# Kernel tuning notes

Hardware: AMD Instinct MI355X
Metric: run time of the kernel (lower is better)

## Reference

```python
import jax, jax.numpy as jnp
import numpy as np
import math

INPUT_SIZE = 512
HIDDEN_SIZE = 1024
BATCH = 64
SEQ = 512


def setup_inputs() -> dict:
    key = jax.random.key(0)
    ks = jax.random.split(key, 13)
    stdv = 1.0 / math.sqrt(HIDDEN_SIZE)
    def u(k, shape):
        return jax.random.uniform(k, shape, jnp.float32, -stdv, stdv)
    x = jax.random.normal(ks[0], (BATCH, SEQ, INPUT_SIZE), jnp.float32)
    return {
        "x": x,
        "U_i": u(ks[1], (INPUT_SIZE, HIDDEN_SIZE)), "V_i": u(ks[2], (HIDDEN_SIZE, HIDDEN_SIZE)), "b_i": u(ks[3], (HIDDEN_SIZE,)),
        "U_f": u(ks[4], (INPUT_SIZE, HIDDEN_SIZE)), "V_f": u(ks[5], (HIDDEN_SIZE, HIDDEN_SIZE)), "b_f": u(ks[6], (HIDDEN_SIZE,)),
        "U_c": u(ks[7], (INPUT_SIZE, HIDDEN_SIZE)), "V_c": u(ks[8], (HIDDEN_SIZE, HIDDEN_SIZE)), "b_c": u(ks[9], (HIDDEN_SIZE,)),
        "U_o": u(ks[10], (INPUT_SIZE, HIDDEN_SIZE)), "V_o": u(ks[11], (HIDDEN_SIZE, HIDDEN_SIZE)), "b_o": u(ks[12], (HIDDEN_SIZE,)),
    }


def reference(x, U_i, V_i, b_i, U_f, V_f, b_f, U_c, V_c, b_c, U_o, V_o, b_o):
    B, T, _ = x.shape
    H = V_i.shape[0]
    # Fuse the four input->gate matmuls into one wide GEMM over all timesteps.
    U = jnp.concatenate([U_i, U_f, U_c, U_o], axis=1)  # [I, 4H]
    V = jnp.concatenate([V_i, V_f, V_c, V_o], axis=1)  # [H, 4H]
    b = jnp.concatenate([b_i, b_f, b_c, b_o], axis=0)  # [4H]
    xU = jnp.einsum('bti,ig->tbg', x, U) + b           # [T, B, 4H]

    def step(carry, xu_t):
        h, c = carry
        gates = xu_t + h @ V                           # [B, 4H]
        i_t = jax.nn.sigmoid(gates[:, 0*H:1*H])
        f_t = jax.nn.sigmoid(gates[:, 1*H:2*H])
        g_t = jax.nn.sigmoid(gates[:, 2*H:3*H])  # NOTE: source uses sigmoid, not tanh
        o_t = jax.nn.sigmoid(gates[:, 3*H:4*H])
        c = f_t * c + i_t * g_t
        h = o_t * jnp.tanh(c)
        return (h, c), h

    h0 = jnp.zeros((B, H), x.dtype)
    c0 = jnp.zeros((B, H), x.dtype)
    (h_T, c_T), hs = jax.lax.scan(step, (h0, c0), xU)
    hidden_seq = jnp.transpose(hs, (1, 0, 2))          # [B, T, H]
    return hidden_seq, (h_T, c_T)
```

## Files before the change

### kernel.cpp

```cpp
#include <hip/hip_runtime.h>
#include <stdint.h>

#define B_  64
#define T_  512
#define I_  512
#define H_  1024
#define G4  4096
#define KW  1536

#define GROUPS 4
#define GBLK   64
#define MBR    16

#define LDS_BYTES 66048

typedef __attribute__((ext_vector_type(8))) short bf16x8;
typedef __attribute__((ext_vector_type(4))) float f32x4;

#define OFF_WT   ((size_t)0)
#define OFF_XB   ((size_t)(16u << 20))
#define OFF_HB   (OFF_XB + (size_t)33554432)
#define WS_NEED  (OFF_HB + (size_t)262144)

__device__ __forceinline__ unsigned short f2bf(float x) {
  unsigned u = __float_as_uint(x);
  u += 0x7FFFu + ((u >> 16) & 1u);
  return (unsigned short)(u >> 16);
}
__device__ __forceinline__ float sigm(float x) {
  return 1.0f / (1.0f + __expf(-x));
}

__global__ __launch_bounds__(256) void pack_w_kernel(
    const float* __restrict__ U0, const float* __restrict__ U1,
    const float* __restrict__ U2, const float* __restrict__ U3,
    const float* __restrict__ V0, const float* __restrict__ V1,
    const float* __restrict__ V2, const float* __restrict__ V3,
    short* __restrict__ Wt)
{
  __shared__ short sl[64][65];
  const int c0 = blockIdx.x * 64;
  const int k0 = blockIdx.y * 64;
  const int g  = c0 >> 10;
  const int h0 = c0 & 1023;
  const float* srcU = (g == 0 ? U0 : g == 1 ? U1 : g == 2 ? U2 : U3);
  const float* srcV = (g == 0 ? V0 : g == 1 ? V1 : g == 2 ? V2 : V3);
  const float* src  = (k0 < 512) ? (srcU + (size_t)k0 * H_)
                                 : (srcV + (size_t)(k0 - 512) * H_);
  const int tid = threadIdx.x;
  const int cl = tid & 63;
  const int r4 = tid >> 6;
  #pragma unroll
  for (int r = 0; r < 16; ++r) {
    const int kl = r * 4 + r4;
    sl[kl][cl] = (short)f2bf(src[(size_t)kl * H_ + h0 + cl]);
  }
  __syncthreads();
  #pragma unroll
  for (int r = 0; r < 16; ++r) {
    const int cl2 = r * 4 + r4;
    Wt[(size_t)(c0 + cl2) * KW + k0 + cl] = sl[cl][cl2];
  }
}

__global__ __launch_bounds__(256) void xcvt(
    const float* __restrict__ x, short* __restrict__ xb)
{
  const int nt = 524288;
  const int idx = blockIdx.x * 256 + threadIdx.x;
  #pragma unroll
  for (int i = 0; i < 8; ++i) {
    const int j = idx + i * nt;
    const float4 v = ((const float4*)x)[j];
    uint2 pk;
    pk.x = (unsigned)f2bf(v.x) | ((unsigned)f2bf(v.y) << 16);
    pk.y = (unsigned)f2bf(v.z) | ((unsigned)f2bf(v.w) << 16);
    ((uint2*)xb)[j] = pk;
  }
}

#define FR_ADDR(unit, slot) ((((unit) * 64) + ((slot) ^ ((unit) & 7))) * 8)

__global__ __launch_bounds__(512, 2) void lstm_rec(
    const short* __restrict__ Wt, const short* __restrict__ xb,
    const float* __restrict__ b0g, const float* __restrict__ b1g,
    const float* __restrict__ b2g, const float* __restrict__ b3g,
    short* __restrict__ hb, float* __restrict__ out)
{
  extern __shared__ char smem[];
  short* sh = (short*)smem;
  short* sx = (short*)(smem + 32768);
  float* gl = (float*)(smem + 49152);

  const int tid = threadIdx.x;
  const int blk = blockIdx.x;
  const int g   = blk >> 6;
  const int bi  = blk & 63;
  const int base = bi * 16;
  const int b0  = g * MBR;

  const int w = tid >> 6, l = tid & 63;
  const int kq = w & 3;
  const int np = w >> 2;
  const int cit = l & 15;
  const int l16 = l >> 4;
  const int slot_r = (cit << 2) | l16;

  bf16x8 vfr[2][8];
  bf16x8 ufr[2][4];
  #pragma unroll
  for (int n = 0; n < 2; ++n) {
    const int col = (np * 2 + n) * 1024 + base + cit;
    const short* wp = Wt + (size_t)col * KW;
    #pragma unroll
    for (int j = 0; j < 8; ++j)
      vfr[n][j] = *(const bf16x8*)(wp + 512 + kq * 256 + j * 32 + l16 * 8);
    #pragma unroll
    for (int j = 0; j < 4; ++j)
      ufr[n][j] = *(const bf16x8*)(wp + kq * 128 + j * 32 + l16 * 8);
  }

  const float* bias0 = (np == 0) ? b0g : b2g;
  const float* bias1 = (np == 0) ? b1g : b3g;
  const float bv0 = (kq == 0) ? bias0[base + cit] : 0.0f;
  const float bv1 = (kq == 0) ? bias1[base + cit] : 0.0f;

  const int crow = tid >> 4;
  const int ccj  = tid & 15;

  const int xr0_row = tid >> 6;
  const int xr1_row = 8 + (tid >> 6);
  const int x_k0 = (tid & 63) * 8;
  const int x_unit = x_k0 >> 5;
  const int xr0_addr = FR_ADDR(x_unit, (xr0_row << 2) | (tid & 3));
  const int xr1_addr = FR_ADDR(x_unit, (xr1_row << 2) | (tid & 3));
  const short* xsrc0 = xb + (size_t)(b0 + xr0_row) * T_ * I_ + x_k0;
  const short* xsrc1 = xb + (size_t)(b0 + xr1_row) * T_ * I_ + x_k0;

  float c_state = 0.0f;

  *(int4*)(sx + xr0_addr) = *(const int4*)(xsrc0);
  *(int4*)(sx + xr1_addr) = *(const int4*)(xsrc1);
  __syncthreads();
  f32x4 xacc0 = (f32x4){bv0, bv0, bv0, bv0};
  f32x4 xacc1 = (f32x4){bv1, bv1, bv1, bv1};
  #pragma unroll
  for (int j = 0; j < 4; ++j) {
    const bf16x8 xf = *(const bf16x8*)(sx + FR_ADDR(kq * 4 + j, slot_r));
    xacc0 = __builtin_amdgcn_mfma_f32_16x16x32_bf16(xf, ufr[0][j], xacc0, 0, 0, 0);
    xacc1 = __builtin_amdgcn_mfma_f32_16x16x32_bf16(xf, ufr[1][j], xacc1, 0, 0, 0);
  }
  int4 xr0 = *(const int4*)(xsrc0 + (size_t)1 * I_);
  int4 xr1 = *(const int4*)(xsrc1 + (size_t)1 * I_);

  for (int t = 0; t < T_; ++t) {
    {
      const unsigned expw = ((t >> 1) & 1) ? 0x00010001u : 0u;
      const short* hsrc = hb + ((size_t)(t & 1) * GROUPS + g) * (MBR * H_);
      int4 v0, v1, v2, v3;
      for (;;) {
        #define LDC(ii, vv) { \
          const short* p = hsrc + (size_t)((((ii) * 512 + tid) >> 7)) * H_ \
                           + ((((ii) * 512 + tid) & 127) * 8); \
          asm volatile("global_load_dwordx4 %0, %1, off sc0 sc1" : "=&v"(vv) : "v"(p)); }
        LDC(0, v0) LDC(1, v1) LDC(2, v2) LDC(3, v3)
        #undef LDC
        asm volatile("s_waitcnt vmcnt(0)" ::: "memory");
        __builtin_amdgcn_sched_barrier(0);
        #define XR(vv) (((unsigned)(vv).x ^ expw) | ((unsigned)(vv).y ^ expw) | \
                        ((unsigned)(vv).z ^ expw) | ((unsigned)(vv).w ^ expw))
        const unsigned diff = (XR(v0) | XR(v1) | XR(v2) | XR(v3)) & 0x00010001u;
        #undef XR
        if (__all(diff == 0u)) break;
        asm volatile("s_sleep 1" ::: "memory");
      }
      #define STC(ii, vv) { const int f = (ii) * 512 + tid; const int row = f >> 7; \
        const int k0s = (f & 127) * 8; \
        *(int4*)(sh + FR_ADDR(k0s >> 5, (row << 2) | ((k0s >> 3) & 3))) = vv; }
      STC(0, v0) STC(1, v1) STC(2, v2) STC(3, v3)
      #undef STC
    }
    __syncthreads();

    f32x4 acc0 = xacc0, acc1 = xacc1;
    #pragma unroll
    for (int j = 0; j < 8; ++j) {
      const bf16x8 af = *(const bf16x8*)(sh + FR_ADDR(kq * 8 + j, slot_r));
      acc0 = __builtin_amdgcn_mfma_f32_16x16x32_bf16(af, vfr[0][j], acc0, 0, 0, 0);
      acc1 = __builtin_amdgcn_mfma_f32_16x16x32_bf16(af, vfr[1][j], acc1, 0, 0, 0);
    }

    #pragma unroll
    for (int i = 0; i < 4; ++i) {
      gl[(l16 * 4 + i) * 260 + kq * 64 + (np * 2 + 0) * 16 + cit] = acc0[i];
      gl[(l16 * 4 + i) * 260 + kq * 64 + (np * 2 + 1) * 16 + cit] = acc1[i];
    }
    __syncthreads();

    if (tid < 256) {
      const float* gr = gl + crow * 260;
      float s[4];
      #pragma unroll
      for (int gate = 0; gate < 4; ++gate)
        s[gate] = gr[0 * 64 + gate * 16 + ccj] + gr[1 * 64 + gate * 16 + ccj]
                + gr[2 * 64 + gate * 16 + ccj] + gr[3 * 64 + gate * 16 + ccj];
      const float i_ = sigm(s[0]), f_ = sigm(s[1]), g_ = sigm(s[2]), o_ = sigm(s[3]);
      c_state = f_ * c_state + i_ * g_;
      const float hval = o_ * tanhf(c_state);
      if (t + 1 < T_) {
        unsigned hv = (unsigned)f2bf(hval);
        hv = (hv & ~1u) | (unsigned)(((t + 1) >> 1) & 1);
        short* hdst = hb + ((size_t)((t + 1) & 1) * GROUPS + g) * (MBR * H_)
                      + (size_t)crow * H_ + base + ccj;
        asm volatile("global_store_short %0, %1, off sc0 sc1" :: "v"(hdst), "v"(hv) : "memory");
      }
      out[((size_t)(b0 + crow) << 19) + (size_t)t * H_ + base + ccj] = hval;
      if (t == T_ - 1) {
        out[(size_t)B_ * T_ * H_ + (size_t)(b0 + crow) * H_ + base + ccj] = hval;
        out[(size_t)B_ * T_ * H_ + (size_t)B_ * H_ + (size_t)(b0 + crow) * H_ + base + ccj] = c_state;
      }
    }

    if (t + 1 < T_) {
      *(int4*)(sx + xr0_addr) = xr0;
      *(int4*)(sx + xr1_addr) = xr1;
      {
        const size_t tn = (size_t)((t + 2 < T_) ? t + 2 : T_ - 1);
        xr0 = *(const int4*)(xsrc0 + tn * I_);
        xr1 = *(const int4*)(xsrc1 + tn * I_);
      }
      __syncthreads();

      xacc0 = (f32x4){bv0, bv0, bv0, bv0};
      xacc1 = (f32x4){bv1, bv1, bv1, bv1};
      #pragma unroll
      for (int j = 0; j < 4; ++j) {
        const bf16x8 xf = *(const bf16x8*)(sx + FR_ADDR(kq * 4 + j, slot_r));
        xacc0 = __builtin_amdgcn_mfma_f32_16x16x32_bf16(xf, ufr[0][j], xacc0, 0, 0, 0);
        xacc1 = __builtin_amdgcn_mfma_f32_16x16x32_bf16(xf, ufr[1][j], xacc1, 0, 0, 0);
      }
    }
  }
}

extern "C" void kernel_launch(void* const* d_in, const int* in_sizes, int n_in,
                              void* d_out, int out_size, void* d_ws, size_t ws_size,
                              hipStream_t stream)
{
  const float* x  = (const float*)d_in[0];
  const float* U0 = (const float*)d_in[1];
  const float* Vg0 = (const float*)d_in[2];
  const float* bg0 = (const float*)d_in[3];
  const float* U1 = (const float*)d_in[4];
  const float* Vg1 = (const float*)d_in[5];
  const float* bg1 = (const float*)d_in[6];
  const float* U2 = (const float*)d_in[7];
  const float* Vg2 = (const float*)d_in[8];
  const float* bg2 = (const float*)d_in[9];
  const float* U3 = (const float*)d_in[10];
  const float* Vg3 = (const float*)d_in[11];
  const float* bg3 = (const float*)d_in[12];

  if (ws_size < WS_NEED) return;

  char* ws = (char*)d_ws;
  short* Wt = (short*)(ws + OFF_WT);
  short* xb = (short*)(ws + OFF_XB);
  short* hb = (short*)(ws + OFF_HB);

  (void)hipFuncSetAttribute((const void*)lstm_rec,
                      hipFuncAttributeMaxDynamicSharedMemorySize, LDS_BYTES);

  (void)hipMemsetAsync(ws + OFF_HB, 0x00, 131072, stream);
  (void)hipMemsetAsync(ws + OFF_HB + 131072, 0x01, 131072, stream);
  pack_w_kernel<<<dim3(64, 24), 256, 0, stream>>>(U0, U1, U2, U3, Vg0, Vg1, Vg2, Vg3, Wt);
  xcvt<<<dim3(2048), 256, 0, stream>>>(x, xb);
  lstm_rec<<<dim3(GROUPS * GBLK), 512, LDS_BYTES, stream>>>(
      Wt, xb, bg0, bg1, bg2, bg3, hb, (float*)d_out);
}
```

Measured before the change: 1.143 ms.

## Give each wave a private h tile to drop the block barrier before MFMA

Each wave now polls and loads only the part of the hidden state its own K-quarter needs, and writes it into a private LDS region. This removes the __syncthreads between the h load and the recurrent MFMA. A single-vector probe spin runs before the bulk eight-load read, and the sleep in the bulk retry grows. tanhf is replaced with an exp-based fast tanh. LDS use grows and the launch bound drops to one block per CU; each wave now loads its share redundantly (2x total h traffic), and fast_tanh may overflow to inf for large inputs.

Result: slower. 1.461 ms (+27.8%).

```diff
diff --git a/kernel.cpp b/kernel.cpp
--- a/kernel.cpp
+++ b/kernel.cpp
@@ -12,7 +12,7 @@
 #define GBLK   64
 #define MBR    16
 
-#define LDS_BYTES 66048
+#define LDS_BYTES 98560
 
 typedef __attribute__((ext_vector_type(8))) short bf16x8;
 typedef __attribute__((ext_vector_type(4))) float f32x4;
@@ -29,6 +29,10 @@
 }
 __device__ __forceinline__ float sigm(float x) {
   return 1.0f / (1.0f + __expf(-x));
+}
+__device__ __forceinline__ float fast_tanh(float x) {
+  const float e2 = __expf(2.0f * x);
+  return 1.0f - 2.0f / (e2 + 1.0f);
 }
 
 __global__ __launch_bounds__(256) void pack_w_kernel(
@@ -81,7 +85,7 @@
 
 #define FR_ADDR(unit, slot) ((((unit) * 64) + ((slot) ^ ((unit) & 7))) * 8)
 
-__global__ __launch_bounds__(512, 2) void lstm_rec(
+__global__ __launch_bounds__(512, 1) void lstm_rec(
     const short* __restrict__ Wt, const short* __restrict__ xb,
     const float* __restrict__ b0g, const float* __restrict__ b1g,
     const float* __restrict__ b2g, const float* __restrict__ b3g,
@@ -89,8 +93,8 @@
 {
   extern __shared__ char smem[];
   short* sh = (short*)smem;
-  short* sx = (short*)(smem + 32768);
-  float* gl = (float*)(smem + 49152);
+  short* sx = (short*)(smem + 65536);
+  float* gl = (float*)(smem + 81920);
 
   const int tid = threadIdx.x;
   const int blk = blockIdx.x;
@@ -105,6 +109,7 @@
   const int cit = l & 15;
   const int l16 = l >> 4;
   const int slot_r = (cit << 2) | l16;
+  short* shw = sh + w * 4096;
 
   bf16x8 vfr[2][8];
   bf16x8 ufr[2][4];
@@ -128,6 +133,11 @@
   const int crow = tid >> 4;
   const int ccj  = tid & 15;
 
+  const int prow = l >> 5;
+  const int pcolo = kq * 256 + (l & 31) * 8;
+  const int s_unit = (l >> 2) & 7;
+  const int s_ks = l & 3;
+
   const int xr0_row = tid >> 6;
   const int xr1_row = 8 + (tid >> 6);
   const int x_k0 = (tid & 63) * 8;
@@ -152,40 +162,51 @@
   }
   int4 xr0 = *(const int4*)(xsrc0 + (size_t)1 * I_);
   int4 xr1 = *(const int4*)(xsrc1 + (size_t)1 * I_);
+  __syncthreads();
 
   for (int t = 0; t < T_; ++t) {
     {
       const unsigned expw = ((t >> 1) & 1) ? 0x00010001u : 0u;
       const short* hsrc = hb + ((size_t)(t & 1) * GROUPS + g) * (MBR * H_);
-      int4 v0, v1, v2, v3;
+      const short* pb = hsrc + (size_t)prow * H_ + pcolo;
+      #define XR(vv) ((((unsigned)(vv).x ^ expw) | ((unsigned)(vv).y ^ expw) | \
+                       ((unsigned)(vv).z ^ expw) | ((unsigned)(vv).w ^ expw)) & 0x00010001u)
+      {
+        int4 pv;
+        for (;;) {
+          asm volatile("global_load_dwordx4 %0, %1, off sc0 sc1" : "=&v"(pv) : "v"(pb));
+          asm volatile("s_waitcnt vmcnt(0)" ::: "memory");
+          if (__all(XR(pv) == 0u)) break;
+          asm volatile("s_sleep 1" ::: "memory");
+        }
+      }
+      int4 v0, v1, v2, v3, v4, v5, v6, v7;
       for (;;) {
         #define LDC(ii, vv) { \
-          const short* p = hsrc + (size_t)((((ii) * 512 + tid) >> 7)) * H_ \
-                           + ((((ii) * 512 + tid) & 127) * 8); \
+          const short* p = hsrc + (size_t)(2 * (ii) + prow) * H_ + pcolo; \
           asm volatile("global_load_dwordx4 %0, %1, off sc0 sc1" : "=&v"(vv) : "v"(p)); }
         LDC(0, v0) LDC(1, v1) LDC(2, v2) LDC(3, v3)
+        LDC(4, v4) LDC(5, v5) LDC(6, v6) LDC(7, v7)
         #undef LDC
         asm volatile("s_waitcnt vmcnt(0)" ::: "memory");
         __builtin_amdgcn_sched_barrier(0);
-        #define XR(vv) (((unsigned)(vv).x ^ expw) | ((unsigned)(vv).y ^ expw) | \
-                        ((unsigned)(vv).z ^ expw) | ((unsigned)(vv).w ^ expw))
-        const unsigned diff = (XR(v0) | XR(v1) | XR(v2) | XR(v3)) & 0x00010001u;
-        #undef XR
+        const unsigned diff = XR(v0) | XR(v1) | XR(v2) | XR(v3)
+                            | XR(v4) | XR(v5) | XR(v6) | XR(v7);
         if (__all(diff == 0u)) break;
-        asm volatile("s_sleep 1" ::: "memory");
-      }
-      #define STC(ii, vv) { const int f = (ii) * 512 + tid; const int row = f >> 7; \
-        const int k0s = (f & 127) * 8; \
-        *(int4*)(sh + FR_ADDR(k0s >> 5, (row << 2) | ((k0s >> 3) & 3))) = vv; }
+        asm volatile("s_sleep 2" ::: "memory");
+      }
+      #undef XR
+      #define STC(ii, vv) { const int row = 2 * (ii) + prow; \
+        *(int4*)(shw + FR_ADDR(s_unit, (row << 2) | s_ks)) = vv; }
       STC(0, v0) STC(1, v1) STC(2, v2) STC(3, v3)
+      STC(4, v4) STC(5, v5) STC(6, v6) STC(7, v7)
       #undef STC
     }
-    __syncthreads();
 
     f32x4 acc0 = xacc0, acc1 = xacc1;
     #pragma unroll
     for (int j = 0; j < 8; ++j) {
-      const bf16x8 af = *(const bf16x8*)(sh + FR_ADDR(kq * 8 + j, slot_r));
+      const bf16x8 af = *(const bf16x8*)(shw + FR_ADDR(j, slot_r));
       acc0 = __builtin_amdgcn_mfma_f32_16x16x32_bf16(af, vfr[0][j], acc0, 0, 0, 0);
       acc1 = __builtin_amdgcn_mfma_f32_16x16x32_bf16(af, vfr[1][j], acc1, 0, 0, 0);
     }
@@ -206,7 +227,7 @@
                 + gr[2 * 64 + gate * 16 + ccj] + gr[3 * 64 + gate * 16 + ccj];
       const float i_ = sigm(s[0]), f_ = sigm(s[1]), g_ = sigm(s[2]), o_ = sigm(s[3]);
       c_state = f_ * c_state + i_ * g_;
-      const float hval = o_ * tanhf(c_state);
+      const float hval = o_ * fast_tanh(c_state);
       if (t + 1 < T_) {
         unsigned hv = (unsigned)f2bf(hval);
         hv = (hv & ~1u) | (unsigned)(((t + 1) >> 1) & 1);
```

## Interleave two batch groups per block with speculative h prefetch and narrower column slices

Applied to the files above, without the earlier changes.

Each block now owns 8 hidden columns for two 16-row batch groups and alternates between them, so the wait on one group's h exchange overlaps with computing the other. The h loads for the next half-step are issued speculatively before the barrier and checked afterwards, with a retry loop if the parity flags do not match. x is loaded straight into registers as MFMA fragments instead of going through LDS, tanh is replaced with an exp-based form, and the K dimension is split across all 8 waves. The kernel now runs at one block per CU with more LDS, and reloading h on a failed speculation costs extra memory traffic.

Result: slower. 3.029 ms (+165.0%).

```diff
diff --git a/kernel.cpp b/kernel.cpp
--- a/kernel.cpp
+++ b/kernel.cpp
@@ -5,14 +5,9 @@
 #define T_  512
 #define I_  512
 #define H_  1024
-#define G4  4096
 #define KW  1536
 
-#define GROUPS 4
-#define GBLK   64
-#define MBR    16
-
-#define LDS_BYTES 66048
+#define LDS_BYTES 98816
 
 typedef __attribute__((ext_vector_type(8))) short bf16x8;
 typedef __attribute__((ext_vector_type(4))) float f32x4;
@@ -29,6 +24,13 @@
 }
 __device__ __forceinline__ float sigm(float x) {
   return 1.0f / (1.0f + __expf(-x));
+}
+__device__ __forceinline__ float fast_tanh(float x) {
+  const float e2 = __expf(2.0f * x);
+  return 1.0f - 2.0f / (e2 + 1.0f);
+}
+__device__ __forceinline__ bf16x8 bc8(int4 v) {
+  union { int4 i; bf16x8 b; } u; u.i = v; return u.b;
 }
 
 __global__ __launch_bounds__(256) void pack_w_kernel(
@@ -80,166 +82,209 @@
 }
 
 #define FR_ADDR(unit, slot) ((((unit) * 64) + ((slot) ^ ((unit) & 7))) * 8)
-
-__global__ __launch_bounds__(512, 2) void lstm_rec(
+#define FOFF(f) ((((f) >> 7) * 1024) + (((f) & 127) * 8))
+#define SADR(f) FR_ADDR((((f) & 127) >> 2), ((((f) >> 7) << 2) | ((f) & 3)))
+
+#define XRD_(vv, ew) ((((unsigned)(vv).x ^ (ew)) | ((unsigned)(vv).y ^ (ew)) | \
+                       ((unsigned)(vv).z ^ (ew)) | ((unsigned)(vv).w ^ (ew))) & 0x00010001u)
+#define LDH(vv, p) asm volatile("global_load_dwordx4 %0, %1, off sc0 sc1" : "=&v"(vv) : "v"(p));
+#define LDX(vv, p) asm volatile("global_load_dwordx4 %0, %1, off" : "=&v"(vv) : "v"(p));
+
+#define RETRY_(hsrc, ew) \
+  for (;;) { \
+    LDH(sp0, (hsrc) + foff0) LDH(sp1, (hsrc) + foff1) \
+    LDH(sp2, (hsrc) + foff2) LDH(sp3, (hsrc) + foff3) \
+    asm volatile("s_waitcnt vmcnt(0)" ::: "memory"); \
+    __builtin_amdgcn_sched_barrier(0); \
+    if (__all((XRD_(sp0, ew) | XRD_(sp1, ew) | XRD_(sp2, ew) | XRD_(sp3, ew)) == 0u)) break; \
+    asm volatile("s_sleep 1" ::: "memory"); \
+  }
+
+#define HALF(SH, GL, HBG, XROW, B0, XACCA, XACCB, CST, HLAST, XVA, XVB, SPECHBG, SPECT, TCUR, DOCHK) \
+{ \
+  const unsigned ew = (((TCUR) >> 1) & 1) ? 0x00010001u : 0u; \
+  const short* hsrc = (HBG) + (((TCUR) & 1) ? 65536 : 0); \
+  bool ok = (DOCHK); \
+  if (ok) { \
+    asm volatile("s_waitcnt vmcnt(2)" ::: "memory"); \
+    __builtin_amdgcn_sched_barrier(0); \
+    ok = __all((XRD_(sp0, ew) | XRD_(sp1, ew) | XRD_(sp2, ew) | XRD_(sp3, ew)) == 0u); \
+  } \
+  if (!ok) { RETRY_(hsrc, ew) } \
+  *(int4*)((SH) + saddr0) = sp0; \
+  *(int4*)((SH) + saddr1) = sp1; \
+  *(int4*)((SH) + saddr2) = sp2; \
+  *(int4*)((SH) + saddr3) = sp3; \
+  { const int tn = ((TCUR) + 1 < T_) ? (TCUR) + 1 : T_ - 1; \
+    const short* xp = (XROW) + (size_t)tn * I_; \
+    LDX(XVA, xp) LDX(XVB, xp + 32) } \
+  { const short* ss = (SPECHBG) + (((SPECT) & 1) ? 65536 : 0); \
+    LDH(sp0, ss + foff0) LDH(sp1, ss + foff1) LDH(sp2, ss + foff2) LDH(sp3, ss + foff3) } \
+  __syncthreads(); \
+  f32x4 accA = XACCA, accB = XACCB; \
+  { \
+    bf16x8 af; \
+    af = *(const bf16x8*)((SH) + FR_ADDR(kqe * 4 + 0, slot_r)); \
+    accA = __builtin_amdgcn_mfma_f32_16x16x32_bf16(af, vfr0[0], accA, 0, 0, 0); \
+    accB = __builtin_amdgcn_mfma_f32_16x16x32_bf16(af, vfr1[0], accB, 0, 0, 0); \
+    af = *(const bf16x8*)((SH) + FR_ADDR(kqe * 4 + 1, slot_r)); \
+    accA = __builtin_amdgcn_mfma_f32_16x16x32_bf16(af, vfr0[1], accA, 0, 0, 0); \
+    accB = __builtin_amdgcn_mfma_f32_16x16x32_bf16(af, vfr1[1], accB, 0, 0, 0); \
+    af = *(const bf16x8*)((SH) + FR_ADDR(kqe * 4 + 2, slot_r)); \
+    accA = __builtin_amdgcn_mfma_f32_16x16x32_bf16(af, vfr0[2], accA, 0, 0, 0); \
+    accB = __builtin_amdgcn_mfma_f32_16x16x32_bf16(af, vfr1[2], accB, 0, 0, 0); \
+    af = *(const bf16x8*)((SH) + FR_ADDR(kqe * 4 + 3, slot_r)); \
+    accA = __builtin_amdgcn_mfma_f32_16x16x32_bf16(af, vfr0[3], accA, 0, 0, 0); \
+    accB = __builtin_amdgcn_mfma_f32_16x16x32_bf16(af, vfr1[3], accB, 0, 0, 0); \
+  } \
+  { \
+    (GL)[(l16 * 4 + 0) * 260 + cit * 8 + kqe] = accA[0]; \
+    (GL)[(l16 * 4 + 1) * 260 + cit * 8 + kqe] = accA[1]; \
+    (GL)[(l16 * 4 + 2) * 260 + cit * 8 + kqe] = accA[2]; \
+    (GL)[(l16 * 4 + 3) * 260 + cit * 8 + kqe] = accA[3]; \
+    (GL)[(l16 * 4 + 0) * 260 + (16 + cit) * 8 + kqe] = accB[0]; \
+    (GL)[(l16 * 4 + 1) * 260 + (16 + cit) * 8 + kqe] = accB[1]; \
+    (GL)[(l16 * 4 + 2) * 260 + (16 + cit) * 8 + kqe] = accB[2]; \
+    (GL)[(l16 * 4 + 3) * 260 + (16 + cit) * 8 + kqe] = accB[3]; \
+  } \
+  __syncthreads(); \
+  asm volatile("s_waitcnt vmcnt(4)" ::: "memory"); \
+  __builtin_amdgcn_sched_barrier(0); \
+  { \
+    const bf16x8 xf0 = bc8(XVA), xf1 = bc8(XVB); \
+    XACCA = (f32x4){bv0, bv0, bv0, bv0}; \
+    XACCB = (f32x4){bv1, bv1, bv1, bv1}; \
+    XACCA = __builtin_amdgcn_mfma_f32_16x16x32_bf16(xf0, ufr0[0], XACCA, 0, 0, 0); \
+    XACCA = __builtin_amdgcn_mfma_f32_16x16x32_bf16(xf1, ufr0[1], XACCA, 0, 0, 0); \
+    XACCB = __builtin_amdgcn_mfma_f32_16x16x32_bf16(xf0, ufr1[0], XACCB, 0, 0, 0); \
+    XACCB = __builtin_amdgcn_mfma_f32_16x16x32_bf16(xf1, ufr1[1], XACCB, 0, 0, 0); \
+  } \
+  if (l < 16) { \
+    const float* gr = (GL) + crow * 260; \
+    const f32x4 a0 = *(const f32x4*)(gr + ccol * 8); \
+    const f32x4 b0a = *(const f32x4*)(gr + ccol * 8 + 4); \
+    const f32x4 a1 = *(const f32x4*)(gr + 64 + ccol * 8); \
+    const f32x4 b1a = *(const f32x4*)(gr + 64 + ccol * 8 + 4); \
+    const f32x4 a2 = *(const f32x4*)(gr + 128 + ccol * 8); \
+    const f32x4 b2a = *(const f32x4*)(gr + 128 + ccol * 8 + 4); \
+    const f32x4 a3 = *(const f32x4*)(gr + 192 + ccol * 8); \
+    const f32x4 b3a = *(const f32x4*)(gr + 192 + ccol * 8 + 4); \
+    const float s0 = a0[0]+a0[1]+a0[2]+a0[3]+b0a[0]+b0a[1]+b0a[2]+b0a[3]; \
+    const float s1 = a1[0]+a1[1]+a1[2]+a1[3]+b1a[0]+b1a[1]+b1a[2]+b1a[3]; \
+    const float s2 = a2[0]+a2[1]+a2[2]+a2[3]+b2a[0]+b2a[1]+b2a[2]+b2a[3]; \
+    const float s3 = a3[0]+a3[1]+a3[2]+a3[3]+b3a[0]+b3a[1]+b3a[2]+b3a[3]; \
+    const float i_ = sigm(s0), f_ = sigm(s1), g_ = sigm(s2), o_ = sigm(s3); \
+    CST = f_ * CST + i_ * g_; \
+    const float hv = o_ * fast_tanh(CST); \
+    HLAST = hv; \
+    unsigned hu = (unsigned)f2bf(hv); \
+    hu = (hu & ~1u) | (unsigned)((((TCUR) + 1) >> 1) & 1); \
+    short* hd = (HBG) + ((((TCUR) + 1) & 1) ? 65536 : 0) + crow * 1024 + base8 + ccol; \
+    asm volatile("global_store_short %0, %1, off sc0 sc1" :: "v"(hd), "v"(hu) : "memory"); \
+    float* op = out + (((size_t)((B0) + crow)) << 19) + (size_t)(TCUR) * H_ + base8 + ccol; \
+    asm volatile("global_store_dword %0, %1, off" :: "v"(op), "v"(hv) : "memory"); \
+  } \
+}
+
+__global__ __launch_bounds__(512, 1) void lstm_rec(
     const short* __restrict__ Wt, const short* __restrict__ xb,
     const float* __restrict__ b0g, const float* __restrict__ b1g,
     const float* __restrict__ b2g, const float* __restrict__ b3g,
     short* __restrict__ hb, float* __restrict__ out)
 {
   extern __shared__ char smem[];
-  short* sh = (short*)smem;
-  short* sx = (short*)(smem + 32768);
-  float* gl = (float*)(smem + 49152);
+  short* shP = (short*)smem;
+  short* shQ = (short*)(smem + 32768);
+  float* glP = (float*)(smem + 65536);
+  float* glQ = (float*)(smem + 82176);
 
   const int tid = threadIdx.x;
   const int blk = blockIdx.x;
-  const int g   = blk >> 6;
-  const int bi  = blk & 63;
-  const int base = bi * 16;
-  const int b0  = g * MBR;
-
+  const int pair = blk >> 7;
+  const int bi = blk & 127;
+  const int base8 = bi * 8;
   const int w = tid >> 6, l = tid & 63;
-  const int kq = w & 3;
-  const int np = w >> 2;
-  const int cit = l & 15;
-  const int l16 = l >> 4;
+  const int kqe = w;
+  const int cit = l & 15, l16 = l >> 4;
   const int slot_r = (cit << 2) | l16;
-
-  bf16x8 vfr[2][8];
-  bf16x8 ufr[2][4];
-  #pragma unroll
-  for (int n = 0; n < 2; ++n) {
-    const int col = (np * 2 + n) * 1024 + base + cit;
-    const short* wp = Wt + (size_t)col * KW;
+  const int Pg = pair * 2, Qg = pair * 2 + 1;
+  const int b0P = Pg * 16, b0Q = Qg * 16;
+
+  short* hbP = hb + Pg * 16384;
+  short* hbQ = hb + Qg * 16384;
+
+  bf16x8 vfr0[4], vfr1[4], ufr0[2], ufr1[2];
+  float bv0, bv1;
+  {
+    const int g0 = cit >> 3, c8 = cit & 7;
+    const short* wpa = Wt + (size_t)(g0 * 1024 + base8 + c8) * KW;
+    const short* wpb = Wt + (size_t)((2 + g0) * 1024 + base8 + c8) * KW;
     #pragma unroll
-    for (int j = 0; j < 8; ++j)
-      vfr[n][j] = *(const bf16x8*)(wp + 512 + kq * 256 + j * 32 + l16 * 8);
+    for (int j = 0; j < 4; ++j) {
+      vfr0[j] = *(const bf16x8*)(wpa + 512 + kqe * 128 + j * 32 + l16 * 8);
+      vfr1[j] = *(const bf16x8*)(wpb + 512 + kqe * 128 + j * 32 + l16 * 8);
+    }
     #pragma unroll
-    for (int j = 0; j < 4; ++j)
-      ufr[n][j] = *(const bf16x8*)(wp + kq * 128 + j * 32 + l16 * 8);
-  }
-
-  const float* bias0 = (np == 0) ? b0g : b2g;
-  const float* bias1 = (np == 0) ? b1g : b3g;
-  const float bv0 = (kq == 0) ? bias0[base + cit] : 0.0f;
-  const float bv1 = (kq == 0) ? bias1[base + cit] : 0.0f;
-
-  const int crow = tid >> 4;
-  const int ccj  = tid & 15;
-
-  const int xr0_row = tid >> 6;
-  const int xr1_row = 8 + (tid >> 6);
-  const int x_k0 = (tid & 63) * 8;
-  const int x_unit = x_k0 >> 5;
-  const int xr0_addr = FR_ADDR(x_unit, (xr0_row << 2) | (tid & 3));
-  const int xr1_addr = FR_ADDR(x_unit, (xr1_row << 2) | (tid & 3));
-  const short* xsrc0 = xb + (size_t)(b0 + xr0_row) * T_ * I_ + x_k0;
-  const short* xsrc1 = xb + (size_t)(b0 + xr1_row) * T_ * I_ + x_k0;
-
-  float c_state = 0.0f;
-
-  *(int4*)(sx + xr0_addr) = *(const int4*)(xsrc0);
-  *(int4*)(sx + xr1_addr) = *(const int4*)(xsrc1);
-  __syncthreads();
-  f32x4 xacc0 = (f32x4){bv0, bv0, bv0, bv0};
-  f32x4 xacc1 = (f32x4){bv1, bv1, bv1, bv1};
-  #pragma unroll
-  for (int j = 0; j < 4; ++j) {
-    const bf16x8 xf = *(const bf16x8*)(sx + FR_ADDR(kq * 4 + j, slot_r));
-    xacc0 = __builtin_amdgcn_mfma_f32_16x16x32_bf16(xf, ufr[0][j], xacc0, 0, 0, 0);
-    xacc1 = __builtin_amdgcn_mfma_f32_16x16x32_bf16(xf, ufr[1][j], xacc1, 0, 0, 0);
-  }
-  int4 xr0 = *(const int4*)(xsrc0 + (size_t)1 * I_);
-  int4 xr1 = *(const int4*)(xsrc1 + (size_t)1 * I_);
+    for (int j = 0; j < 2; ++j) {
+      ufr0[j] = *(const bf16x8*)(wpa + kqe * 64 + j * 32 + l16 * 8);
+      ufr1[j] = *(const bf16x8*)(wpb + kqe * 64 + j * 32 + l16 * 8);
+    }
+    const float* bpa = g0 ? b1g : b0g;
+    const float* bpb = g0 ? b3g : b2g;
+    bv0 = (kqe == 0) ? bpa[base8 + c8] : 0.0f;
+    bv1 = (kqe == 0) ? bpb[base8 + c8] : 0.0f;
+  }
+
+  const int f0_ = tid, f1_ = 512 + tid, f2_ = 1024 + tid, f3_ = 1536 + tid;
+  const int foff0 = FOFF(f0_), foff1 = FOFF(f1_), foff2 = FOFF(f2_), foff3 = FOFF(f3_);
+  const int saddr0 = SADR(f0_), saddr1 = SADR(f1_), saddr2 = SADR(f2_), saddr3 = SADR(f3_);
+
+  const short* xrowP = xb + (size_t)(b0P + cit) * T_ * I_ + kqe * 64 + l16 * 8;
+  const short* xrowQ = xb + (size_t)(b0Q + cit) * T_ * I_ + kqe * 64 + l16 * 8;
+
+  const int crow = 2 * w + (l >> 3);
+  const int ccol = l & 7;
+
+  float cP = 0.0f, cQ = 0.0f, hlP = 0.0f, hlQ = 0.0f;
+  int4 sp0, sp1, sp2, sp3;
+  int4 xvP0, xvP1, xvQ0, xvQ1;
+  f32x4 xaccP0, xaccP1, xaccQ0, xaccQ1;
+
+  LDX(xvP0, xrowP) LDX(xvP1, xrowP + 32)
+  LDX(xvQ0, xrowQ) LDX(xvQ1, xrowQ + 32)
+  asm volatile("s_waitcnt vmcnt(0)" ::: "memory");
+  __builtin_amdgcn_sched_barrier(0);
+  {
+    const bf16x8 p0 = bc8(xvP0), p1 = bc8(xvP1), q0 = bc8(xvQ0), q1 = bc8(xvQ1);
+    xaccP0 = (f32x4){bv0, bv0, bv0, bv0};
+    xaccP1 = (f32x4){bv1, bv1, bv1, bv1};
+    xaccQ0 = (f32x4){bv0, bv0, bv0, bv0};
+    xaccQ1 = (f32x4){bv1, bv1, bv1, bv1};
+    xaccP0 = __builtin_amdgcn_mfma_f32_16x16x32_bf16(p0, ufr0[0], xaccP0, 0, 0, 0);
+    xaccP0 = __builtin_amdgcn_mfma_f32_16x16x32_bf16(p1, ufr0[1], xaccP0, 0, 0, 0);
+    xaccP1 = __builtin_amdgcn_mfma_f32_16x16x32_bf16(p0, ufr1[0], xaccP1, 0, 0, 0);
+    xaccP1 = __builtin_amdgcn_mfma_f32_16x16x32_bf16(p1, ufr1[1], xaccP1, 0, 0, 0);
+    xaccQ0 = __builtin_amdgcn_mfma_f32_16x16x32_bf16(q0, ufr0[0], xaccQ0, 0, 0, 0);
+    xaccQ0 = __builtin_amdgcn_mfma_f32_16x16x32_bf16(q1, ufr0[1], xaccQ0, 0, 0, 0);
+    xaccQ1 = __builtin_amdgcn_mfma_f32_16x16x32_bf16(q0, ufr1[0], xaccQ1, 0, 0, 0);
+    xaccQ1 = __builtin_amdgcn_mfma_f32_16x16x32_bf16(q1, ufr1[1], xaccQ1, 0, 0, 0);
+  }
 
   for (int t = 0; t < T_; ++t) {
-    {
-      const unsigned expw = ((t >> 1) & 1) ? 0x00010001u : 0u;
-      const short* hsrc = hb + ((size_t)(t & 1) * GROUPS + g) * (MBR * H_);
-      int4 v0, v1, v2, v3;
-      for (;;) {
-        #define LDC(ii, vv) { \
-          const short* p = hsrc + (size_t)((((ii) * 512 + tid) >> 7)) * H_ \
-                           + ((((ii) * 512 + tid) & 127) * 8); \
-          asm volatile("global_load_dwordx4 %0, %1, off sc0 sc1" : "=&v"(vv) : "v"(p)); }
-        LDC(0, v0) LDC(1, v1) LDC(2, v2) LDC(3, v3)
-        #undef LDC
-        asm volatile("s_waitcnt vmcnt(0)" ::: "memory");
-        __builtin_amdgcn_sched_barrier(0);
-        #define XR(vv) (((unsigned)(vv).x ^ expw) | ((unsigned)(vv).y ^ expw) | \
-                        ((unsigned)(vv).z ^ expw) | ((unsigned)(vv).w ^ expw))
-        const unsigned diff = (XR(v0) | XR(v1) | XR(v2) | XR(v3)) & 0x00010001u;
-        #undef XR
-        if (__all(diff == 0u)) break;
-        asm volatile("s_sleep 1" ::: "memory");
-      }
-      #define STC(ii, vv) { const int f = (ii) * 512 + tid; const int row = f >> 7; \
-        const int k0s = (f & 127) * 8; \
-        *(int4*)(sh + FR_ADDR(k0s >> 5, (row << 2) | ((k0s >> 3) & 3))) = vv; }
-      STC(0, v0) STC(1, v1) STC(2, v2) STC(3, v3)
-      #undef STC
-    }
-    __syncthreads();
-
-    f32x4 acc0 = xacc0, acc1 = xacc1;
-    #pragma unroll
-    for (int j = 0; j < 8; ++j) {
-      const bf16x8 af = *(const bf16x8*)(sh + FR_ADDR(kq * 8 + j, slot_r));
-      acc0 = __builtin_amdgcn_mfma_f32_16x16x32_bf16(af, vfr[0][j], acc0, 0, 0, 0);
-      acc1 = __builtin_amdgcn_mfma_f32_16x16x32_bf16(af, vfr[1][j], acc1, 0, 0, 0);
-    }
-
-    #pragma unroll
-    for (int i = 0; i < 4; ++i) {
-      gl[(l16 * 4 + i) * 260 + kq * 64 + (np * 2 + 0) * 16 + cit] = acc0[i];
-      gl[(l16 * 4 + i) * 260 + kq * 64 + (np * 2 + 1) * 16 + cit] = acc1[i];
-    }
-    __syncthreads();
-
-    if (tid < 256) {
-      const float* gr = gl + crow * 260;
-      float s[4];
-      #pragma unroll
-      for (int gate = 0; gate < 4; ++gate)
-        s[gate] = gr[0 * 64 + gate * 16 + ccj] + gr[1 * 64 + gate * 16 + ccj]
-                + gr[2 * 64 + gate * 16 + ccj] + gr[3 * 64 + gate * 16 + ccj];
-      const float i_ = sigm(s[0]), f_ = sigm(s[1]), g_ = sigm(s[2]), o_ = sigm(s[3]);
-      c_state = f_ * c_state + i_ * g_;
-      const float hval = o_ * tanhf(c_state);
-      if (t + 1 < T_) {
-        unsigned hv = (unsigned)f2bf(hval);
-        hv = (hv & ~1u) | (unsigned)(((t + 1) >> 1) & 1);
-        short* hdst = hb + ((size_t)((t + 1) & 1) * GROUPS + g) * (MBR * H_)
-                      + (size_t)crow * H_ + base + ccj;
-        asm volatile("global_store_short %0, %1, off sc0 sc1" :: "v"(hdst), "v"(hv) : "memory");
-      }
-      out[((size_t)(b0 + crow) << 19) + (size_t)t * H_ + base + ccj] = hval;
-      if (t == T_ - 1) {
-        out[(size_t)B_ * T_ * H_ + (size_t)(b0 + crow) * H_ + base + ccj] = hval;
-        out[(size_t)B_ * T_ * H_ + (size_t)B_ * H_ + (size_t)(b0 + crow) * H_ + base + ccj] = c_state;
-      }
-    }
-
-    if (t + 1 < T_) {
-      *(int4*)(sx + xr0_addr) = xr0;
-      *(int4*)(sx + xr1_addr) = xr1;
-      {
-        const size_t tn = (size_t)((t + 2 < T_) ? t + 2 : T_ - 1);
-        xr0 = *(const int4*)(xsrc0 + tn * I_);
-        xr1 = *(const int4*)(xsrc1 + tn * I_);
-      }
-      __syncthreads();
-
-      xacc0 = (f32x4){bv0, bv0, bv0, bv0};
-      xacc1 = (f32x4){bv1, bv1, bv1, bv1};
-      #pragma unroll
-      for (int j = 0; j < 4; ++j) {
-        const bf16x8 xf = *(const bf16x8*)(sx + FR_ADDR(kq * 4 + j, slot_r));
-        xacc0 = __builtin_amdgcn_mfma_f32_16x16x32_bf16(xf, ufr[0][j], xacc0, 0, 0, 0);
-        xacc1 = __builtin_amdgcn_mfma_f32_16x16x32_bf16(xf, ufr[1][j], xacc1, 0, 0, 0);
-      }
-    }
+    HALF(shP, glP, hbP, xrowP, b0P, xaccP0, xaccP1, cP, hlP, xvP0, xvP1, hbQ, t,     t, (t > 0))
+    HALF(shQ, glQ, hbQ, xrowQ, b0Q, xaccQ0, xaccQ1, cQ, hlQ, xvQ0, xvQ1, hbP, t + 1, t, true)
+  }
+
+  if (l < 16) {
+    const size_t fb = (size_t)B_ * T_ * H_;
+    float* p1 = out + fb + (size_t)(b0P + crow) * H_ + base8 + ccol;
+    float* p2 = out + fb + (size_t)B_ * H_ + (size_t)(b0P + crow) * H_ + base8 + ccol;
+    float* q1 = out + fb + (size_t)(b0Q + crow) * H_ + base8 + ccol;
+    float* q2 = out + fb + (size_t)B_ * H_ + (size_t)(b0Q + crow) * H_ + base8 + ccol;
+    asm volatile("global_store_dword %0, %1, off" :: "v"(p1), "v"(hlP) : "memory");
+    asm volatile("global_store_dword %0, %1, off" :: "v"(p2), "v"(cP) : "memory");
+    asm volatile("global_store_dword %0, %1, off" :: "v"(q1), "v"(hlQ) : "memory");
+    asm volatile("global_store_dword %0, %1, off" :: "v"(q2), "v"(cQ) : "memory");
   }
 }
 
@@ -275,6 +320,6 @@
   (void)hipMemsetAsync(ws + OFF_HB + 131072, 0x01, 131072, stream);
   pack_w_kernel<<<dim3(64, 24), 256, 0, stream>>>(U0, U1, U2, U3, Vg0, Vg1, Vg2, Vg3, Wt);
   xcvt<<<dim3(2048), 256, 0, stream>>>(x, xb);
-  lstm_rec<<<dim3(GROUPS * GBLK), 512, LDS_BYTES, stream>>>(
+  lstm_rec<<<dim3(256), 512, LDS_BYTES, stream>>>(
       Wt, xb, bg0, bg1, bg2, bg3, hb, (float*)d_out);
 }
```

## Halve recurrent block count with 32 hidden columns per block and faster gate reduction

Applied to the files above, without the earlier changes.

Each block now owns 32 hidden columns instead of 16, so the grid shrinks from 256 to 128 persistent blocks and each wave holds four weight-fragment sets in registers and issues four MFMA chains per step. The gate scratch layout is transposed so that all 512 threads do the cell update, each reading its four partial sums with one vector load. tanh is replaced by an exp-based approximation. The intent is to cut the number of blocks polling the global h buffer and spread per-step elementwise work over more threads. In exchange it doubles VGPR use for weights, raises LDS to about 82 KB, and could reduce occupancy or cause spills under launch_bounds(512,2).

Result: slower. 3.113 ms (+172.3%).

```diff
diff --git a/kernel.cpp b/kernel.cpp
--- a/kernel.cpp
+++ b/kernel.cpp
@@ -9,10 +9,10 @@
 #define KW  1536
 
 #define GROUPS 4
-#define GBLK   64
+#define GBLK   32
 #define MBR    16
 
-#define LDS_BYTES 66048
+#define LDS_BYTES 82432
 
 typedef __attribute__((ext_vector_type(8))) short bf16x8;
 typedef __attribute__((ext_vector_type(4))) float f32x4;
@@ -29,6 +29,10 @@
 }
 __device__ __forceinline__ float sigm(float x) {
   return 1.0f / (1.0f + __expf(-x));
+}
+__device__ __forceinline__ float fast_tanh(float x) {
+  const float e2 = __expf(2.0f * x);
+  return 1.0f - 2.0f / (e2 + 1.0f);
 }
 
 __global__ __launch_bounds__(256) void pack_w_kernel(
@@ -81,6 +85,8 @@
 
 #define FR_ADDR(unit, slot) ((((unit) * 64) + ((slot) ^ ((unit) & 7))) * 8)
 
+#define MFMA_ __builtin_amdgcn_mfma_f32_16x16x32_bf16
+
 __global__ __launch_bounds__(512, 2) void lstm_rec(
     const short* __restrict__ Wt, const short* __restrict__ xb,
     const float* __restrict__ b0g, const float* __restrict__ b1g,
@@ -94,9 +100,9 @@
 
   const int tid = threadIdx.x;
   const int blk = blockIdx.x;
-  const int g   = blk >> 6;
-  const int bi  = blk & 63;
-  const int base = bi * 16;
+  const int g   = blk >> 5;
+  const int bi  = blk & 31;
+  const int base = bi * 32;
   const int b0  = g * MBR;
 
   const int w = tid >> 6, l = tid & 63;
@@ -106,27 +112,40 @@
   const int l16 = l >> 4;
   const int slot_r = (cit << 2) | l16;
 
-  bf16x8 vfr[2][8];
-  bf16x8 ufr[2][4];
-  #pragma unroll
-  for (int n = 0; n < 2; ++n) {
-    const int col = (np * 2 + n) * 1024 + base + cit;
-    const short* wp = Wt + (size_t)col * KW;
+  bf16x8 vfr0[8], vfr1[8], vfr2[8], vfr3[8];
+  bf16x8 ufr0[4], ufr1[4], ufr2[4], ufr3[4];
+  {
+    const int g0_ = np * 2, g1_ = np * 2 + 1;
+    const short* wp0 = Wt + (size_t)(g0_ * 1024 + base + cit) * KW;
+    const short* wp1 = Wt + (size_t)(g0_ * 1024 + base + 16 + cit) * KW;
+    const short* wp2 = Wt + (size_t)(g1_ * 1024 + base + cit) * KW;
+    const short* wp3 = Wt + (size_t)(g1_ * 1024 + base + 16 + cit) * KW;
     #pragma unroll
-    for (int j = 0; j < 8; ++j)
-      vfr[n][j] = *(const bf16x8*)(wp + 512 + kq * 256 + j * 32 + l16 * 8);
+    for (int j = 0; j < 8; ++j) {
+      const int o = 512 + kq * 256 + j * 32 + l16 * 8;
+      vfr0[j] = *(const bf16x8*)(wp0 + o);
+      vfr1[j] = *(const bf16x8*)(wp1 + o);
+      vfr2[j] = *(const bf16x8*)(wp2 + o);
+      vfr3[j] = *(const bf16x8*)(wp3 + o);
+    }
     #pragma unroll
-    for (int j = 0; j < 4; ++j)
-      ufr[n][j] = *(const bf16x8*)(wp + kq * 128 + j * 32 + l16 * 8);
-  }
-
-  const float* bias0 = (np == 0) ? b0g : b2g;
-  const float* bias1 = (np == 0) ? b1g : b3g;
-  const float bv0 = (kq == 0) ? bias0[base + cit] : 0.0f;
-  const float bv1 = (kq == 0) ? bias1[base + cit] : 0.0f;
-
-  const int crow = tid >> 4;
-  const int ccj  = tid & 15;
+    for (int j = 0; j < 4; ++j) {
+      const int o = kq * 128 + j * 32 + l16 * 8;
+      ufr0[j] = *(const bf16x8*)(wp0 + o);
+      ufr1[j] = *(const bf16x8*)(wp1 + o);
+      ufr2[j] = *(const bf16x8*)(wp2 + o);
+      ufr3[j] = *(const bf16x8*)(wp3 + o);
+    }
+  }
+  const float* bp0 = (np == 0) ? b0g : b2g;
+  const float* bp1 = (np == 0) ? b1g : b3g;
+  const float bv0 = (kq == 0) ? bp0[base + cit] : 0.0f;
+  const float bv1 = (kq == 0) ? bp0[base + 16 + cit] : 0.0f;
+  const float bv2 = (kq == 0) ? bp1[base + cit] : 0.0f;
+  const float bv3 = (kq == 0) ? bp1[base + 16 + cit] : 0.0f;
+
+  const int crow = tid >> 5;
+  const int ccol = tid & 31;
 
   const int xr0_row = tid >> 6;
   const int xr1_row = 8 + (tid >> 6);
@@ -142,13 +161,17 @@
   *(int4*)(sx + xr0_addr) = *(const int4*)(xsrc0);
   *(int4*)(sx + xr1_addr) = *(const int4*)(xsrc1);
   __syncthreads();
-  f32x4 xacc0 = (f32x4){bv0, bv0, bv0, bv0};
-  f32x4 xacc1 = (f32x4){bv1, bv1, bv1, bv1};
+  f32x4 xa0 = (f32x4){bv0, bv0, bv0, bv0};
+  f32x4 xa1 = (f32x4){bv1, bv1, bv1, bv1};
+  f32x4 xa2 = (f32x4){bv2, bv2, bv2, bv2};
+  f32x4 xa3 = (f32x4){bv3, bv3, bv3, bv3};
   #pragma unroll
   for (int j = 0; j < 4; ++j) {
     const bf16x8 xf = *(const bf16x8*)(sx + FR_ADDR(kq * 4 + j, slot_r));
-    xacc0 = __builtin_amdgcn_mfma_f32_16x16x32_bf16(xf, ufr[0][j], xacc0, 0, 0, 0);
-    xacc1 = __builtin_amdgcn_mfma_f32_16x16x32_bf16(xf, ufr[1][j], xacc1, 0, 0, 0);
+    xa0 = MFMA_(xf, ufr0[j], xa0, 0, 0, 0);
+    xa1 = MFMA_(xf, ufr1[j], xa1, 0, 0, 0);
+    xa2 = MFMA_(xf, ufr2[j], xa2, 0, 0, 0);
+    xa3 = MFMA_(xf, ufr3[j], xa3, 0, 0, 0);
   }
   int4 xr0 = *(const int4*)(xsrc0 + (size_t)1 * I_);
   int4 xr1 = *(const int4*)(xsrc1 + (size_t)1 * I_);
@@ -182,42 +205,53 @@
     }
     __syncthreads();
 
-    f32x4 acc0 = xacc0, acc1 = xacc1;
+    f32x4 a0 = xa0, a1 = xa1, a2 = xa2, a3 = xa3;
     #pragma unroll
     for (int j = 0; j < 8; ++j) {
       const bf16x8 af = *(const bf16x8*)(sh + FR_ADDR(kq * 8 + j, slot_r));
-      acc0 = __builtin_amdgcn_mfma_f32_16x16x32_bf16(af, vfr[0][j], acc0, 0, 0, 0);
-      acc1 = __builtin_amdgcn_mfma_f32_16x16x32_bf16(af, vfr[1][j], acc1, 0, 0, 0);
-    }
-
-    #pragma unroll
-    for (int i = 0; i < 4; ++i) {
-      gl[(l16 * 4 + i) * 260 + kq * 64 + (np * 2 + 0) * 16 + cit] = acc0[i];
-      gl[(l16 * 4 + i) * 260 + kq * 64 + (np * 2 + 1) * 16 + cit] = acc1[i];
+      a0 = MFMA_(af, vfr0[j], a0, 0, 0, 0);
+      a1 = MFMA_(af, vfr1[j], a1, 0, 0, 0);
+      a2 = MFMA_(af, vfr2[j], a2, 0, 0, 0);
+      a3 = MFMA_(af, vfr3[j], a3, 0, 0, 0);
+    }
+
+    {
+      const int g0_ = np * 2, g1_ = np * 2 + 1;
+      #pragma unroll
+      for (int e = 0; e < 4; ++e) {
+        const int rr = (l16 * 4 + e) * 520;
+        gl[rr + (g0_ * 32 + cit) * 4 + kq]      = a0[e];
+        gl[rr + (g0_ * 32 + 16 + cit) * 4 + kq] = a1[e];
+        gl[rr + (g1_ * 32 + cit) * 4 + kq]      = a2[e];
+        gl[rr + (g1_ * 32 + 16 + cit) * 4 + kq] = a3[e];
+      }
     }
     __syncthreads();
 
-    if (tid < 256) {
-      const float* gr = gl + crow * 260;
-      float s[4];
-      #pragma unroll
-      for (int gate = 0; gate < 4; ++gate)
-        s[gate] = gr[0 * 64 + gate * 16 + ccj] + gr[1 * 64 + gate * 16 + ccj]
-                + gr[2 * 64 + gate * 16 + ccj] + gr[3 * 64 + gate * 16 + ccj];
-      const float i_ = sigm(s[0]), f_ = sigm(s[1]), g_ = sigm(s[2]), o_ = sigm(s[3]);
+    {
+      const float* gr = gl + crow * 520;
+      const f32x4 si = *(const f32x4*)(gr + (0 * 32 + ccol) * 4);
+      const f32x4 sf = *(const f32x4*)(gr + (1 * 32 + ccol) * 4);
+      const f32x4 sg = *(const f32x4*)(gr + (2 * 32 + ccol) * 4);
+      const f32x4 so = *(const f32x4*)(gr + (3 * 32 + ccol) * 4);
+      const float s0 = si[0] + si[1] + si[2] + si[3];
+      const float s1 = sf[0] + sf[1] + sf[2] + sf[3];
+      const float s2 = sg[0] + sg[1] + sg[2] + sg[3];
+      const float s3 = so[0] + so[1] + so[2] + so[3];
+      const float i_ = sigm(s0), f_ = sigm(s1), g_ = sigm(s2), o_ = sigm(s3);
       c_state = f_ * c_state + i_ * g_;
-      const float hval = o_ * tanhf(c_state);
+      const float hval = o_ * fast_tanh(c_state);
       if (t + 1 < T_) {
         unsigned hv = (unsigned)f2bf(hval);
         hv = (hv & ~1u) | (unsigned)(((t + 1) >> 1) & 1);
         short* hdst = hb + ((size_t)((t + 1) & 1) * GROUPS + g) * (MBR * H_)
-                      + (size_t)crow * H_ + base + ccj;
+                      + (size_t)crow * H_ + base + ccol;
         asm volatile("global_store_short %0, %1, off sc0 sc1" :: "v"(hdst), "v"(hv) : "memory");
       }
-      out[((size_t)(b0 + crow) << 19) + (size_t)t * H_ + base + ccj] = hval;
+      out[((size_t)(b0 + crow) << 19) + (size_t)t * H_ + base + ccol] = hval;
       if (t == T_ - 1) {
-        out[(size_t)B_ * T_ * H_ + (size_t)(b0 + crow) * H_ + base + ccj] = hval;
-        out[(size_t)B_ * T_ * H_ + (size_t)B_ * H_ + (size_t)(b0 + crow) * H_ + base + ccj] = c_state;
+        out[(size_t)B_ * T_ * H_ + (size_t)(b0 + crow) * H_ + base + ccol] = hval;
+        out[(size_t)B_ * T_ * H_ + (size_t)B_ * H_ + (size_t)(b0 + crow) * H_ + base + ccol] = c_state;
       }
     }
 
@@ -231,13 +265,17 @@
       }
       __syncthreads();
 
-      xacc0 = (f32x4){bv0, bv0, bv0, bv0};
-      xacc1 = (f32x4){bv1, bv1, bv1, bv1};
+      xa0 = (f32x4){bv0, bv0, bv0, bv0};
+      xa1 = (f32x4){bv1, bv1, bv1, bv1};
+      xa2 = (f32x4){bv2, bv2, bv2, bv2};
+      xa3 = (f32x4){bv3, bv3, bv3, bv3};
       #pragma unroll
       for (int j = 0; j < 4; ++j) {
         const bf16x8 xf = *(const bf16x8*)(sx + FR_ADDR(kq * 4 + j, slot_r));
-        xacc0 = __builtin_amdgcn_mfma_f32_16x16x32_bf16(xf, ufr[0][j], xacc0, 0, 0, 0);
-        xacc1 = __builtin_amdgcn_mfma_f32_16x16x32_bf16(xf, ufr[1][j], xacc1, 0, 0, 0);
+        xa0 = MFMA_(xf, ufr0[j], xa0, 0, 0, 0);
+        xa1 = MFMA_(xf, ufr1[j], xa1, 0, 0, 0);
+        xa2 = MFMA_(xf, ufr2[j], xa2, 0, 0, 0);
+        xa3 = MFMA_(xf, ufr3[j], xa3, 0, 0, 0);
       }
     }
   }
```
